# Performance work log

Hardware: AMD Instinct MI355X
Metric: run time of the kernel (lower is better)

The kernel has to match this reference:

```python
import jax, jax.numpy as jnp
import numpy as np

FEATURE_MAPS = [38, 19, 10, 5, 3, 1]
NUM_ANCHORS = [4, 6, 6, 6, 4, 4]
SCALE_RANGE = (0.1, 0.9)
RATIO_RANGE = (0.5, 2.0)
BACKGROUND_ID = 0
EPS = 1e-6


def make_anchors():
    # Replicates AnchorManager._generate_anchors: for each level, loop i (rows -> cy),
    # j (cols -> cx), then zip(scales, ratios) anchor shapes. Returns [A, 4] cxcywh.
    all_a = []
    for size, na in zip(FEATURE_MAPS, NUM_ANCHORS):
        scales = np.linspace(SCALE_RANGE[0], SCALE_RANGE[1], na)
        ratios = np.linspace(RATIO_RANGE[0], RATIO_RANGE[1], na)
        rs = np.sqrt(ratios)
        w = scales * rs
        h = scales / rs
        c = (np.arange(size) + 0.5) / size
        cy_g, cx_g = np.meshgrid(c, c, indexing='ij')  # i -> cy, j -> cx
        centers = np.stack([cx_g.ravel(), cy_g.ravel()], axis=-1)  # [size*size, 2]
        wh = np.stack([w, h], axis=-1)  # [na, 2]
        a = np.concatenate([np.repeat(centers, na, axis=0), np.tile(wh, (size * size, 1))], axis=1)
        all_a.append(a)
    return np.concatenate(all_a).astype(np.float32)  # [8732, 4]


def _cxcywh_to_xyxy(b):
    return jnp.concatenate([b[..., :2] - b[..., 2:] * 0.5, b[..., :2] + b[..., 2:] * 0.5], axis=-1)


def _pairwise_iou(a, b):
    # a: [B, A, 4] xyxy, b: [B, N, 4] xyxy -> [B, A, N]
    lt = jnp.maximum(a[:, :, None, :2], b[:, None, :, :2])
    rb = jnp.minimum(a[:, :, None, 2:], b[:, None, :, 2:])
    wh = jnp.clip(rb - lt, 0.0)
    inter = wh[..., 0] * wh[..., 1]
    area_a = (a[..., 2] - a[..., 0]) * (a[..., 3] - a[..., 1])
    area_b = (b[..., 2] - b[..., 0]) * (b[..., 3] - b[..., 1])
    union = area_a[:, :, None] + area_b[:, None, :] - inter
    return inter / jnp.maximum(union, EPS)


def setup_inputs() -> dict:
    key = jax.random.key(0)
    k1, k2 = jax.random.split(key)
    B, N = 32, 100
    gt_boxes = jax.random.uniform(k1, (B, N, 4), dtype=jnp.float32)
    gt_labels = jax.random.randint(k2, (B, N), 0, 81, dtype=jnp.int32)
    mask = jnp.ones((B, N), dtype=bool)
    anchors = jnp.asarray(make_anchors())
    return {"gt_boxes": gt_boxes, "gt_labels": gt_labels, "mask": mask, "anchors": anchors}


def reference(gt_boxes, gt_labels, mask, anchors):
    B, N, _ = gt_boxes.shape
    A = anchors.shape[0]
    anc = jnp.broadcast_to(anchors, (B, A, 4))
    anc_xyxy = _cxcywh_to_xyxy(anc)
    ious = _pairwise_iou(anc_xyxy, gt_boxes)  # [B, A, N]

    best_gt_iou = ious.max(axis=-1)          # [B, A]
    best_gt_idx = ious.argmax(axis=-1)       # [B, A]
    best_anchor_idx = ious.argmax(axis=-2)   # [B, N]

    bidx = jnp.arange(B)[:, None]
    best_gt_idx = best_gt_idx.at[bidx, best_anchor_idx].set(jnp.broadcast_to(jnp.arange(N), (B, N)))
    best_gt_iou = best_gt_iou.at[bidx, best_anchor_idx].set(2.0)

    pos_mask = best_gt_iou > 0.5  # [B, A]

    matched_gtb = jnp.take_along_axis(gt_boxes, best_gt_idx[..., None], axis=1)  # [B, A, 4]
    matched_lab = jnp.take_along_axis(gt_labels, best_gt_idx, axis=1)           # [B, A]

    ex = (matched_gtb[..., 0] - anc[..., 0]) / anc[..., 2]
    ey = (matched_gtb[..., 1] - anc[..., 1]) / anc[..., 3]
    ew = jnp.log((matched_gtb[..., 2] + EPS) / (anc[..., 2] + EPS))
    eh = jnp.log((matched_gtb[..., 3] + EPS) / (anc[..., 3] + EPS))
    encoded = jnp.stack([ex, ey, ew, eh], axis=-1)  # [B, A, 4]

    encoded_labels = jnp.where(pos_mask, matched_lab, jnp.int32(BACKGROUND_ID))

    # Batches with no valid GT keep zeros / background (the `continue` branch)
    any_valid = mask.any(axis=-1)  # [B]
    encoded = jnp.where(any_valid[:, None, None], encoded, 0.0)
    encoded_labels = jnp.where(any_valid[:, None], encoded_labels, jnp.int32(BACKGROUND_ID))
    return encoded, encoded_labels, pos_mask
```

## Files before the change

kernel.cpp:

```cpp
#include <hip/hip_runtime.h>

#define A_ 8732
#define B_ 32
#define N_ 100
#define ABLK 35
#define GB_G 4
#define GMAX 25
#define EPSF 1e-6f


__global__ __launch_bounds__(256) void k_pre(
    const float* __restrict__ gt, const float* __restrict__ anchors,
    float4* __restrict__ axyxy, float* __restrict__ aarea,
    float4* __restrict__ cbox, float* __restrict__ carea,
    int* __restrict__ cn, int* __restrict__ cnt, int* __restrict__ win) {
  int tid = threadIdx.x;
  if (blockIdx.x < ABLK) {
    int i = blockIdx.x * 256 + tid;
    if (i < A_) {
      float4 an = ((const float4*)anchors)[i];
      float ax0 = an.x - an.z * 0.5f, ay0 = an.y - an.w * 0.5f;
      float ax1 = an.x + an.z * 0.5f, ay1 = an.y + an.w * 0.5f;
      axyxy[i] = make_float4(ax0, ay0, ax1, ay1);
      aarea[i] = (ax1 - ax0) * (ay1 - ay0);
    }
    return;
  }
  __shared__ int s_cnt[B_];
  if (tid < B_) s_cnt[tid] = 0;
  __syncthreads();
  for (int j = tid; j < B_ * N_; j += 256) {
    win[j] = 0;
    const float* g = gt + (size_t)j * 4;
    float bx0 = g[0], by0 = g[1], bx1 = g[2], by1 = g[3];
    if (bx1 > bx0 && by1 > by0) {
      int b = j / N_;
      int p = atomicAdd(&s_cnt[b], 1);
      cbox[b * N_ + p] = make_float4(bx0, by0, bx1, by1);
      carea[b * N_ + p] = (bx1 - bx0) * (by1 - by0);
      cn[b * N_ + p] = j - b * N_;
    }
  }
  __syncthreads();
  if (tid < B_) cnt[tid] = s_cnt[tid];
}

__global__ __launch_bounds__(256) void k_scan(
    const float4* __restrict__ axyxy, const float* __restrict__ aarea,
    const float4* __restrict__ cbox, const float* __restrict__ carea,
    const int* __restrict__ cn, const int* __restrict__ cnt,
    unsigned long long* __restrict__ partial, int* __restrict__ win) {
  int tid = threadIdx.x;
  int b = blockIdx.x / GMAX;
  int g = blockIdx.x % GMAX;
  int c = cnt[b];
  if (GB_G * g >= c) return;
  __shared__ unsigned long long sred[256];

  float gx0[GB_G], gy0[GB_G], gx1[GB_G], gy1[GB_G], gar[GB_G];
  int gn[GB_G];
  bool live[GB_G];
#pragma unroll
  for (int j = 0; j < GB_G; j++) {
    int p = GB_G * g + j;
    live[j] = p < c;
    int ps = live[j] ? p : 0;
    float4 gb = cbox[b * N_ + ps];
    if (!live[j]) gb = make_float4(1.0f, 1.0f, 0.0f, 0.0f);
    gx0[j] = gb.x; gy0[j] = gb.y; gx1[j] = gb.z; gy1[j] = gb.w;
    gar[j] = carea[b * N_ + ps];
    gn[j] = live[j] ? cn[b * N_ + ps] : 0;
  }
  unsigned long long wkey[GB_G];
#pragma unroll
  for (int j = 0; j < GB_G; j++)
    wkey[j] = (unsigned long long)(0xFFFFFFFFu - (unsigned)tid);

  unsigned long long* prow = partial + ((size_t)b * GMAX + g) * A_;
  for (int a = tid; a < A_; a += 256) {
    float4 axy = axyxy[a];
    float area_a = aarea[a];
    unsigned long long pk = 0ull;
#pragma unroll
    for (int j = 0; j < GB_G; j++) {
      float lx = fmaxf(axy.x, gx0[j]), ly = fmaxf(axy.y, gy0[j]);
      float rx = fminf(axy.z, gx1[j]), ry = fminf(axy.w, gy1[j]);
      float w = fmaxf(rx - lx, 0.0f), h = fmaxf(ry - ly, 0.0f);
      float inter = w * h;
      if (inter > 0.0f) {
        float uni = area_a + gar[j] - inter;
        float iou = inter / fmaxf(uni, EPSF);
        unsigned long long hi = ((unsigned long long)__float_as_uint(iou)) << 32;
        unsigned long long kA = hi | (unsigned long long)(unsigned)(N_ - 1 - gn[j]);
        if (kA > pk) pk = kA;
        unsigned long long kB = hi | (unsigned long long)(0xFFFFFFFFu - (unsigned)a);
        if (kB > wkey[j]) wkey[j] = kB;
      }
    }
    prow[a] = pk;
  }

#pragma unroll
  for (int j = 0; j < GB_G; j++) {
    sred[tid] = wkey[j];
    __syncthreads();
    for (int s = 128; s > 0; s >>= 1) {
      if (tid < s) {
        unsigned long long o = sred[tid + s];
        if (o > sred[tid]) sred[tid] = o;
      }
      __syncthreads();
    }
    if (tid == 0 && live[j])
      win[b * N_ + gn[j]] =
          (int)(0xFFFFFFFFu - (unsigned)(sred[0] & 0xFFFFFFFFull));
    __syncthreads();
  }
}

__global__ __launch_bounds__(256) void k_finalize(
    const float* __restrict__ gt, const int* __restrict__ labels,
    const float* __restrict__ anchors, const unsigned char* __restrict__ mask,
    const unsigned long long* __restrict__ partial, const int* __restrict__ cnt,
    const int* __restrict__ win, float* __restrict__ out) {
  int b = blockIdx.y;
  int a0 = blockIdx.x * 256;
  int tid = threadIdx.x;
  int a = a0 + tid;

  __shared__ int s_ov[256];
  __shared__ int s_any;
  if (tid == 0) s_any = 0;
  s_ov[tid] = -1;
  __syncthreads();
  if (tid < N_) {
    int aw = win[b * N_ + tid];
    if (aw >= a0 && aw < a0 + 256) atomicMax(&s_ov[aw - a0], tid);
  }
  if (tid < 25) {
    unsigned v = ((const unsigned*)mask)[b * 25 + tid];
    if (v) atomicOr(&s_any, 1);
  }
  __syncthreads();
  if (a >= A_) return;

  int G = (cnt[b] + GB_G - 1) / GB_G;
  unsigned long long k = (unsigned long long)(unsigned)(N_ - 1);
  const unsigned long long* prow = partial + (size_t)b * GMAX * A_ + a;
  for (int g = 0; g < G; g++) {
    unsigned long long t = prow[(size_t)g * A_];
    if (t > k) k = t;
  }
  float iou = __uint_as_float((unsigned)(k >> 32));
  int gi = (N_ - 1) - (int)(k & 0xFFFFFFFFull);

  int ov = s_ov[tid];
  bool pos;
  if (ov >= 0) {
    gi = ov;
    pos = true;
  } else {
    pos = iou > 0.5f;
  }

  float4 an = ((const float4*)anchors)[a];
  const float* g = gt + (size_t)(b * N_ + gi) * 4;
  float gx = g[0], gy = g[1], gw = g[2], gh = g[3];

  float ex = (gx - an.x) / an.z;
  float ey = (gy - an.y) / an.w;
  float ew = logf((gw + EPSF) / (an.z + EPSF));
  float eh = logf((gh + EPSF) / (an.w + EPSF));
  int lab = pos ? labels[b * N_ + gi] : 0;

  if (!s_any) { ex = 0.0f; ey = 0.0f; ew = 0.0f; eh = 0.0f; lab = 0; }

  const long long BA = (long long)B_ * A_;
  ((float4*)out)[(size_t)b * A_ + a] = make_float4(ex, ey, ew, eh);
  out[4 * BA + (size_t)b * A_ + a] = (float)lab;
  out[5 * BA + (size_t)b * A_ + a] = pos ? 1.0f : 0.0f;
}

extern "C" void kernel_launch(void* const* d_in, const int* in_sizes, int n_in,
                              void* d_out, int out_size, void* d_ws,
                              size_t ws_size, hipStream_t stream) {
  const float* gt = (const float*)d_in[0];
  const int* labels = (const int*)d_in[1];
  const unsigned char* mask = (const unsigned char*)d_in[2];
  const float* anchors = (const float*)d_in[3];
  float* out = (float*)d_out;

  unsigned long long* partial = (unsigned long long*)d_ws;
  float4* axyxy = (float4*)(partial + (size_t)B_ * GMAX * A_);
  float4* cbox = axyxy + A_;
  float* aarea = (float*)(cbox + B_ * N_);
  float* carea = aarea + A_;
  int* cn = (int*)(carea + B_ * N_);
  int* cnt = cn + B_ * N_;
  int* win = cnt + B_;

  k_pre<<<ABLK + 1, 256, 0, stream>>>(gt, anchors, axyxy, aarea, cbox, carea,
                                      cn, cnt, win);
  k_scan<<<B_ * GMAX, 256, 0, stream>>>(axyxy, aarea, cbox, carea, cn, cnt,
                                        partial, win);
  k_finalize<<<dim3(ABLK, B_), 256, 0, stream>>>(gt, labels, anchors, mask,
                                                 partial, cnt, win, out);
}
```

Measured before the change: 97.32 us.

## Split anchor scan across blocks and merge per-GT argmax in finalize

The scan kernel now splits the anchor range into 8 slices, so each (batch, GT-group) pair is covered by 8 blocks instead of one. Each slice writes its own per-GT best-anchor key to a workspace array, and the finalize kernel reduces those keys for each valid GT. Anchor xyxy and area are now computed inside the scan instead of in a precompute pass, which shrinks k_pre to a single block and removes the win initialisation. This raises parallelism and GPU occupancy for the scan, at the cost of more blocks, repeated block reductions per slice, and extra reads in finalize.

New measurement: 87.36 us. 10.2% less time.

```diff
diff --git a/kernel.cpp b/kernel.cpp
--- a/kernel.cpp
+++ b/kernel.cpp
@@ -6,38 +6,25 @@
 #define ABLK 35
 #define GB_G 4
 #define GMAX 25
+#define SPLIT 8
+#define SLEN 1092
 #define EPSF 1e-6f
 
 
 __global__ __launch_bounds__(256) void k_pre(
-    const float* __restrict__ gt, const float* __restrict__ anchors,
-    float4* __restrict__ axyxy, float* __restrict__ aarea,
-    float4* __restrict__ cbox, float* __restrict__ carea,
-    int* __restrict__ cn, int* __restrict__ cnt, int* __restrict__ win) {
+    const float* __restrict__ gt, float4* __restrict__ cbox,
+    float* __restrict__ carea, int* __restrict__ cn, int* __restrict__ cnt) {
+  __shared__ int s_cnt[B_];
   int tid = threadIdx.x;
-  if (blockIdx.x < ABLK) {
-    int i = blockIdx.x * 256 + tid;
-    if (i < A_) {
-      float4 an = ((const float4*)anchors)[i];
-      float ax0 = an.x - an.z * 0.5f, ay0 = an.y - an.w * 0.5f;
-      float ax1 = an.x + an.z * 0.5f, ay1 = an.y + an.w * 0.5f;
-      axyxy[i] = make_float4(ax0, ay0, ax1, ay1);
-      aarea[i] = (ax1 - ax0) * (ay1 - ay0);
-    }
-    return;
-  }
-  __shared__ int s_cnt[B_];
   if (tid < B_) s_cnt[tid] = 0;
   __syncthreads();
   for (int j = tid; j < B_ * N_; j += 256) {
-    win[j] = 0;
-    const float* g = gt + (size_t)j * 4;
-    float bx0 = g[0], by0 = g[1], bx1 = g[2], by1 = g[3];
-    if (bx1 > bx0 && by1 > by0) {
+    float4 gb = ((const float4*)gt)[j];
+    if (gb.z > gb.x && gb.w > gb.y) {
       int b = j / N_;
       int p = atomicAdd(&s_cnt[b], 1);
-      cbox[b * N_ + p] = make_float4(bx0, by0, bx1, by1);
-      carea[b * N_ + p] = (bx1 - bx0) * (by1 - by0);
+      cbox[b * N_ + p] = gb;
+      carea[b * N_ + p] = (gb.z - gb.x) * (gb.w - gb.y);
       cn[b * N_ + p] = j - b * N_;
     }
   }
@@ -46,13 +33,16 @@
 }
 
 __global__ __launch_bounds__(256) void k_scan(
-    const float4* __restrict__ axyxy, const float* __restrict__ aarea,
-    const float4* __restrict__ cbox, const float* __restrict__ carea,
-    const int* __restrict__ cn, const int* __restrict__ cnt,
-    unsigned long long* __restrict__ partial, int* __restrict__ win) {
+    const float* __restrict__ anchors, const float4* __restrict__ cbox,
+    const float* __restrict__ carea, const int* __restrict__ cn,
+    const int* __restrict__ cnt, unsigned long long* __restrict__ partial,
+    unsigned long long* __restrict__ wsplit) {
   int tid = threadIdx.x;
-  int b = blockIdx.x / GMAX;
-  int g = blockIdx.x % GMAX;
+  int bid = blockIdx.x;
+  int s = bid % SPLIT;
+  int t = bid / SPLIT;
+  int g = t % GMAX;
+  int b = t / GMAX;
   int c = cnt[b];
   if (GB_G * g >= c) return;
   __shared__ unsigned long long sred[256];
@@ -71,20 +61,26 @@
     gar[j] = carea[b * N_ + ps];
     gn[j] = live[j] ? cn[b * N_ + ps] : 0;
   }
+
+  int s0 = s * SLEN;
+  int send = (s0 + SLEN < A_) ? (s0 + SLEN) : A_;
+
   unsigned long long wkey[GB_G];
 #pragma unroll
   for (int j = 0; j < GB_G; j++)
-    wkey[j] = (unsigned long long)(0xFFFFFFFFu - (unsigned)tid);
+    wkey[j] = (unsigned long long)(0xFFFFFFFFu - (unsigned)(s0 + tid));
 
   unsigned long long* prow = partial + ((size_t)b * GMAX + g) * A_;
-  for (int a = tid; a < A_; a += 256) {
-    float4 axy = axyxy[a];
-    float area_a = aarea[a];
+  for (int a = s0 + tid; a < send; a += 256) {
+    float4 an = ((const float4*)anchors)[a];
+    float ax0 = an.x - an.z * 0.5f, ay0 = an.y - an.w * 0.5f;
+    float ax1 = an.x + an.z * 0.5f, ay1 = an.y + an.w * 0.5f;
+    float area_a = (ax1 - ax0) * (ay1 - ay0);
     unsigned long long pk = 0ull;
 #pragma unroll
     for (int j = 0; j < GB_G; j++) {
-      float lx = fmaxf(axy.x, gx0[j]), ly = fmaxf(axy.y, gy0[j]);
-      float rx = fminf(axy.z, gx1[j]), ry = fminf(axy.w, gy1[j]);
+      float lx = fmaxf(ax0, gx0[j]), ly = fmaxf(ay0, gy0[j]);
+      float rx = fminf(ax1, gx1[j]), ry = fminf(ay1, gy1[j]);
       float w = fmaxf(rx - lx, 0.0f), h = fmaxf(ry - ly, 0.0f);
       float inter = w * h;
       if (inter > 0.0f) {
@@ -104,16 +100,15 @@
   for (int j = 0; j < GB_G; j++) {
     sred[tid] = wkey[j];
     __syncthreads();
-    for (int s = 128; s > 0; s >>= 1) {
-      if (tid < s) {
-        unsigned long long o = sred[tid + s];
+    for (int r = 128; r > 0; r >>= 1) {
+      if (tid < r) {
+        unsigned long long o = sred[tid + r];
         if (o > sred[tid]) sred[tid] = o;
       }
       __syncthreads();
     }
     if (tid == 0 && live[j])
-      win[b * N_ + gn[j]] =
-          (int)(0xFFFFFFFFu - (unsigned)(sred[0] & 0xFFFFFFFFull));
+      wsplit[((size_t)b * SPLIT + s) * N_ + gn[j]] = sred[0];
     __syncthreads();
   }
 }
@@ -121,8 +116,9 @@
 __global__ __launch_bounds__(256) void k_finalize(
     const float* __restrict__ gt, const int* __restrict__ labels,
     const float* __restrict__ anchors, const unsigned char* __restrict__ mask,
-    const unsigned long long* __restrict__ partial, const int* __restrict__ cnt,
-    const int* __restrict__ win, float* __restrict__ out) {
+    const unsigned long long* __restrict__ partial,
+    const unsigned long long* __restrict__ wsplit,
+    const int* __restrict__ cnt, float* __restrict__ out) {
   int b = blockIdx.y;
   int a0 = blockIdx.x * 256;
   int tid = threadIdx.x;
@@ -134,7 +130,18 @@
   s_ov[tid] = -1;
   __syncthreads();
   if (tid < N_) {
-    int aw = win[b * N_ + tid];
+    float4 gb = ((const float4*)gt)[b * N_ + tid];
+    int aw = 0;
+    if (gb.z > gb.x && gb.w > gb.y) {
+      const unsigned long long* wp = wsplit + (size_t)b * SPLIT * N_ + tid;
+      unsigned long long k = wp[0];
+#pragma unroll
+      for (int s2 = 1; s2 < SPLIT; s2++) {
+        unsigned long long tk = wp[(size_t)s2 * N_];
+        if (tk > k) k = tk;
+      }
+      aw = (int)(0xFFFFFFFFu - (unsigned)(k & 0xFFFFFFFFull));
+    }
     if (aw >= a0 && aw < a0 + 256) atomicMax(&s_ov[aw - a0], tid);
   }
   if (tid < 25) {
@@ -147,9 +154,9 @@
   int G = (cnt[b] + GB_G - 1) / GB_G;
   unsigned long long k = (unsigned long long)(unsigned)(N_ - 1);
   const unsigned long long* prow = partial + (size_t)b * GMAX * A_ + a;
-  for (int g = 0; g < G; g++) {
-    unsigned long long t = prow[(size_t)g * A_];
-    if (t > k) k = t;
+  for (int g2 = 0; g2 < G; g2++) {
+    unsigned long long t2 = prow[(size_t)g2 * A_];
+    if (t2 > k) k = t2;
   }
   float iou = __uint_as_float((unsigned)(k >> 32));
   int gi = (N_ - 1) - (int)(k & 0xFFFFFFFFull);
@@ -191,18 +198,15 @@
   float* out = (float*)d_out;
 
   unsigned long long* partial = (unsigned long long*)d_ws;
-  float4* axyxy = (float4*)(partial + (size_t)B_ * GMAX * A_);
-  float4* cbox = axyxy + A_;
-  float* aarea = (float*)(cbox + B_ * N_);
-  float* carea = aarea + A_;
+  unsigned long long* wsplit = partial + (size_t)B_ * GMAX * A_;
+  float4* cbox = (float4*)(wsplit + (size_t)B_ * SPLIT * N_);
+  float* carea = (float*)(cbox + B_ * N_);
   int* cn = (int*)(carea + B_ * N_);
   int* cnt = cn + B_ * N_;
-  int* win = cnt + B_;
-
-  k_pre<<<ABLK + 1, 256, 0, stream>>>(gt, anchors, axyxy, aarea, cbox, carea,
-                                      cn, cnt, win);
-  k_scan<<<B_ * GMAX, 256, 0, stream>>>(axyxy, aarea, cbox, carea, cn, cnt,
-                                        partial, win);
+
+  k_pre<<<1, 256, 0, stream>>>(gt, cbox, carea, cn, cnt);
+  k_scan<<<B_ * GMAX * SPLIT, 256, 0, stream>>>(anchors, cbox, carea, cn, cnt,
+                                                partial, wsplit);
   k_finalize<<<dim3(ABLK, B_), 256, 0, stream>>>(gt, labels, anchors, mask,
-                                                 partial, cnt, win, out);
-}
+                                                 partial, wsplit, cnt, out);
+}
```
